# Kernel tuning notes

Measured on AMD Instinct MI355X. Metric: run time of the kernel, lower is better.

## Reference

```python
import jax, jax.numpy as jnp
import numpy as np

N, E = 50000, 800000
D_IN, D_DEG, D_MSG, D_UP, D_H = 128, 16, 128, 128, 256
D = D_IN + D_DEG          # 144, node feature after degree-tag concat
MSG_IN = 2 * D            # 288
UPD_IN = D + D_MSG        # 272

def _mlp_params(key, d_in, d_h, d_out):
    k1, k2 = jax.random.split(key)
    s1 = 1.0 / np.sqrt(d_in)
    s2 = 1.0 / np.sqrt(d_h)
    return (jax.random.uniform(k1, (d_in, d_h), jnp.float32, -s1, s1),
            jnp.zeros((d_h,), jnp.float32),
            jax.random.uniform(k2, (d_h, d_out), jnp.float32, -s2, s2),
            jnp.zeros((d_out,), jnp.float32))

def setup_inputs() -> dict:
    key = jax.random.key(0)
    kx, ke, kd, km, ku = jax.random.split(key, 5)
    x = jax.random.normal(kx, (N, D_IN), jnp.float32)
    edge_index = jax.random.randint(ke, (2, E), 0, N, jnp.int64)
    degrees = jax.random.uniform(kd, (N, D_DEG), jnp.float32)
    mW1, mb1, mW2, mb2 = _mlp_params(km, MSG_IN, D_H, D_MSG)
    uW1, ub1, uW2, ub2 = _mlp_params(ku, UPD_IN, D_H, D_UP)
    return {"x": x, "edge_index": edge_index, "degrees": degrees,
            "msg_W1": mW1, "msg_b1": mb1, "msg_W2": mW2, "msg_b2": mb2,
            "upd_W1": uW1, "upd_b1": ub1, "upd_W2": uW2, "upd_b2": ub2}

def _mlp(h, W1, b1, W2, b2):
    return jax.nn.relu(h @ W1 + b1) @ W2 + b2

def reference(x, edge_index, degrees,
              msg_W1, msg_b1, msg_W2, msg_b2,
              upd_W1, upd_b1, upd_W2, upd_b2):
    # degree_as_tag + retain_features -> concat node features with degree tags
    h = jnp.concatenate([x, degrees], axis=-1)          # [N, D]
    # flow='source_to_target': i = edge_index[1] (target), j = edge_index[0] (source)
    src, tgt = edge_index[0], edge_index[1]
    h_i = h[tgt]                                        # [E, D]
    h_j = h[src]                                        # [E, D]
    msgs = _mlp(jnp.concatenate([h_i, h_j], axis=-1),   # [E, 2D] -> [E, D_MSG]
                msg_W1, msg_b1, msg_W2, msg_b2)
    # sparse sum over source dim == scatter-add onto targets
    agg = jax.ops.segment_sum(msgs, tgt, num_segments=N)  # [N, D_MSG]
    out = _mlp(jnp.concatenate([h, agg], axis=-1),
               upd_W1, upd_b1, upd_W2, upd_b2)          # [N, D_UP]
    return out
```

## Files before the change

kernel.cpp:

```cpp
#include <hip/hip_runtime.h>


#define N_NODES 50000
#define E_EDGES 800000
#define DF   144
#define DIN  128
#define DDEG 16
#define DMSG 128
#define SA_LD 296
#define SH_LD 264
#define PQ_LD 512
#define KA_LD 168
#define EP_W  68
#define ECAP 96
#define OVER_CAP 4096
#define PQ_BLOCKS 782
#define HIST_BLOCKS 3125
#define PACK_THREADS 27648
#define PREP_BLOCKS 3516
#define PACK_BLOCKS 108

typedef __attribute__((ext_vector_type(8))) short short8;
typedef __attribute__((ext_vector_type(4))) float floatx4;
typedef __attribute__((ext_vector_type(4))) unsigned int uintx4;

__device__ __forceinline__ unsigned int fasu(float f){
  union { float f; unsigned int u; } v; v.f = f; return v.u;
}
__device__ __forceinline__ float uasf(unsigned int u){
  union { unsigned int u; float f; } v; v.u = u; return v.f;
}
__device__ __forceinline__ short f2bf(float f){
  unsigned int i = fasu(f);
  unsigned int r = i + 0x7fffu + ((i >> 16) & 1u);
  return (short)(r >> 16);
}
__device__ __forceinline__ unsigned int pk_trunc(float lo, float hi){
  return __builtin_amdgcn_perm(fasu(hi), fasu(lo), 0x07060302u);
}

__global__ void sentinel_kernel(float* __restrict__ out){
  int i = blockIdx.x * blockDim.x + threadIdx.x;
  if (i < N_NODES * DMSG){ out[i] = 2.0f; }
}

__device__ __forceinline__ void pack_w_dev(const float* __restrict__ W,
                                           short* __restrict__ Wp,
                                           int Ksrc, int nT, int t){
  int lane = t & 63;
  int rest = t >> 6;
  int nt = rest % nT;
  int chunk = rest / nT;
  int Ncols = nT * 16;
  int n = nt * 16 + (lane & 15);
  int kbase = chunk * 32 + (lane >> 4) * 8;
  short8 v;
  for (int j = 0; j < 8; ++j){
    int k = kbase + j;
    short o = 0;
    if (k < Ksrc){ o = f2bf(W[(size_t)k * Ncols + n]); }
    v[j] = o;
  }
  *(short8*)(Wp + (size_t)t * 8) = v;
}
__device__ __forceinline__ void pack_w1pq_dev(const float* __restrict__ W1,
                                              short* __restrict__ Wp, int t){
  int lane = t & 63;
  int rest = t >> 6;
  int nt = rest % 32;
  int chunk = rest / 32;
  int col = nt * 16 + (lane & 15);
  int kbase = chunk * 32 + (lane >> 4) * 8;
  short8 v;
  for (int j = 0; j < 8; ++j){
    int k = kbase + j;
    short o = 0;
    if (k < 144){
      float w = (col < 256) ? W1[(size_t)k * 256 + col]
                            : W1[(size_t)(144 + k) * 256 + (col - 256)];
      o = f2bf(w);
    }
    v[j] = o;
  }
  *(short8*)(Wp + (size_t)t * 8) = v;
}

__global__ void prep_pack_kernel(const float* __restrict__ x, const float* __restrict__ deg,
                                 const float* __restrict__ mW1, const float* __restrict__ mW2,
                                 const float* __restrict__ uW1, const float* __restrict__ uW2,
                                 short* __restrict__ w1pq, short* __restrict__ w2m,
                                 short* __restrict__ w1u, short* __restrict__ w2u,
                                 int* __restrict__ cnt, int* __restrict__ nOver,
                                 short* __restrict__ h){
  if (blockIdx.x >= PREP_BLOCKS){
    int t2 = (blockIdx.x - PREP_BLOCKS) * 256 + threadIdx.x;
    if (t2 < 4096){ pack_w_dev(mW2, w2m, 256, 8, t2); }
    else if (t2 < 13312){ pack_w_dev(uW1, w1u, 272, 16, t2 - 4096); }
    else if (t2 < 17408){ pack_w_dev(uW2, w2u, 256, 8, t2 - 13312); }
    else { pack_w1pq_dev(mW1, w1pq, t2 - 17408); }
    return;
  }
  int i = blockIdx.x * 256 + threadIdx.x;
  if (i < N_NODES){ cnt[i] = 0; }
  if (i == 0){ *nOver = 0; }
  if (i < N_NODES * 18){
    int n = i / 18;
    int j = i - n * 18;
    const float* src;
    if (j < 16){ src = x + (size_t)n * DIN + (size_t)j * 8; }
    else       { src = deg + (size_t)n * DDEG + (size_t)(j - 16) * 8; }
    short8 v;
    for (int t = 0; t < 8; ++t){ v[t] = f2bf(src[t]); }
    *(short8*)(h + (size_t)n * DF + (size_t)j * 8) = v;
  }
}

__launch_bounds__(256, 2)
__global__ void pq_scatter_kernel(const short* __restrict__ h, const short* __restrict__ w1pq,
                                  const float* __restrict__ b1, short* __restrict__ PQ,
                                  const int* __restrict__ ei, int* __restrict__ cnt,
                                  int* __restrict__ nOver, unsigned int* __restrict__ over,
                                  unsigned short* __restrict__ es){
  __shared__ __align__(16) unsigned int sE[4 * 32 * EP_W];

  const int g = blockIdx.x;
  const bool isG = ((g % 5) == 0) && ((g / 5) < PQ_BLOCKS);
  if (!isG){
    int nb = (g / 5) + 1; if (nb > PQ_BLOCKS) nb = PQ_BLOCKS;
    int e = (g - nb) * 256 + threadIdx.x;
    if (e < E_EDGES){
      int s = ei[e];
      int t = ei[E_EDGES + e];
      if ((unsigned)s >= (unsigned)N_NODES) s = 0;
      if ((unsigned)t >= (unsigned)N_NODES) t = 0;
      int r = atomicAdd(cnt + t, 1);
      if (r < ECAP){
        es[(size_t)t * ECAP + r] = (unsigned short)s;
      } else {
        int p = atomicAdd(nOver, 1);
        if (p < OVER_CAP){ over[p] = ((unsigned int)t << 16) | (unsigned int)s; }
      }
    }
    return;
  }

  const int tid  = threadIdx.x;
  const int lane = tid & 63;
  const int wave = tid >> 6;
  const int q    = lane >> 4;
  const int lr   = lane & 15;
  const int n0   = (g / 5) * 64;
  short* sA = (short*)sE;

  {
    int row = tid >> 2;
    int quarter = tid & 3;
    int n = n0 + row;
    if (n >= N_NODES) n = 0;
    const short* hp = h + (size_t)n * DF;
    short* dstp = sA + row * KA_LD + quarter * 40;
    #pragma unroll
    for (int c5 = 0; c5 < 5; ++c5){
      int col = quarter * 40 + c5 * 8;
      short8 v;
      if (col < DF){
        v = *(const short8*)(hp + col);
      } else {
        for (int j = 0; j < 8; ++j){ v[j] = 0; }
      }
      *(short8*)(dstp + c5 * 8) = v;
    }
  }
  __syncthreads();

  floatx4 acc[4][8];
  #pragma unroll
  for (int it = 0; it < 4; ++it){
    #pragma unroll
    for (int jt = 0; jt < 8; ++jt){
      #pragma unroll
      for (int r = 0; r < 4; ++r){ acc[it][jt][r] = 0.0f; }
    }
  }

  for (int kc = 0; kc < 5; ++kc){
    short8 aF[4];
    #pragma unroll
    for (int it = 0; it < 4; ++it){
      aF[it] = *(const short8*)(sA + (it * 16 + lr) * KA_LD + kc * 32 + q * 8);
    }
    #pragma unroll
    for (int jt = 0; jt < 8; ++jt){
      short8 bF = *(const short8*)(w1pq + ((size_t)(kc * 32 + wave * 8 + jt) * 64 + lane) * 8);
      #pragma unroll
      for (int it = 0; it < 4; ++it){
        acc[it][jt] = __builtin_amdgcn_mfma_f32_16x16x32_bf16(aF[it], bF, acc[it][jt], 0, 0, 0);
      }
    }
  }
  __syncthreads();

  const int waveBase = wave * (32 * EP_W);
  #pragma unroll
  for (int rnd = 0; rnd < 2; ++rnd){
    #pragma unroll
    for (int il = 0; il < 2; ++il){
      const int it = rnd * 2 + il;
      #pragma unroll
      for (int jt = 0; jt < 8; ++jt){
        int col  = (wave * 8 + jt) * 16 + lr;
        float bb = (col < 256) ? b1[col] : 0.0f;
        floatx4 a = acc[it][jt];
        unsigned int pk01 = pk_trunc(a[0] + bb, a[1] + bb);
        unsigned int pk23 = pk_trunc(a[2] + bb, a[3] + bb);
        unsigned int send = (lr & 1) ? pk01 : pk23;
        unsigned int t = (unsigned int)__shfl_xor((int)send, 1, 64);
        int lrow;
        unsigned int w0, w1;
        if ((lr & 1) == 0){
          lrow = il * 16 + q * 4;
          w0 = (pk01 & 0xffffu) | ((t & 0xffffu) << 16);
          w1 = (pk01 >> 16)     | (t & 0xffff0000u);
        } else {
          lrow = il * 16 + q * 4 + 2;
          w0 = (t & 0xffffu) | ((pk23 & 0xffffu) << 16);
          w1 = (t >> 16)     | (pk23 & 0xffff0000u);
        }
        int wv = jt * 8 + (lr >> 1);
        sE[waveBase + lrow * EP_W + wv] = w0;
        sE[waveBase + (lrow + 1) * EP_W + wv] = w1;
      }
    }
    #pragma unroll
    for (int rr = 0; rr < 8; ++rr){
      int lrow = rr * 4 + (lane >> 4);
      int grow = n0 + rnd * 32 + lrow;
      uintx4 v = *(const uintx4*)(sE + waveBase + lrow * EP_W + (lane & 15) * 4);
      if (grow < N_NODES){
        *(uintx4*)((unsigned int*)PQ + (size_t)grow * 256 + wave * 64 + (lane & 15) * 4) = v;
      }
    }
  }
}

__launch_bounds__(256, 8)
__global__ void hsum_kernel(const short* __restrict__ PQ, const unsigned short* __restrict__ es,
                            const int* __restrict__ cnt, const unsigned int* __restrict__ over,
                            const int* __restrict__ nOver, short* __restrict__ HsumB){
  const int lane = threadIdx.x & 63;
  const int wave = threadIdx.x >> 6;
  const int t = blockIdx.x * 4 + wave;
  const unsigned int* PQu = (const unsigned int*)PQ;

  float a0 = 0.0f, a1 = 0.0f, a2 = 0.0f, a3 = 0.0f;
  int d = cnt[t];
  if (d > 0){
    int dc = d < ECAP ? d : ECAP;
    int start = t * ECAP;
    uint2 pv = *(const uint2*)(PQu + (size_t)t * 256 + lane * 2);
    float Pf0 = uasf(pv.x << 16), Pf1 = uasf(pv.x & 0xffff0000u);
    float Pf2 = uasf(pv.y << 16), Pf3 = uasf(pv.y & 0xffff0000u);

    #define LDQ(idx) (*(const uint2*)(PQu + (size_t)(unsigned int)__shfl((int)el, (idx), 64) * 256 + 128 + lane * 2))
    #define ACCQ(qv) { float v;                                        \
        v = Pf0 + uasf((qv).x << 16);          a0 += v > 0.0f ? v : 0.0f; \
        v = Pf1 + uasf((qv).x & 0xffff0000u);  a1 += v > 0.0f ? v : 0.0f; \
        v = Pf2 + uasf((qv).y << 16);          a2 += v > 0.0f ? v : 0.0f; \
        v = Pf3 + uasf((qv).y & 0xffff0000u);  a3 += v > 0.0f ? v : 0.0f; }

    for (int base = 0; base < dc; base += 64){
      int m = dc - base;
      if (m > 64) m = 64;
      unsigned int el = (lane < m) ? (unsigned int)es[start + base + lane] : 0u;
      uint2 q0 = LDQ(0);
      uint2 q1 = LDQ(1);
      uint2 q2 = LDQ(2);
      uint2 q3 = LDQ(3);
      for (int j = 0; j < m; j += 4){
        uint2 t0 = q0, t1 = q1, t2 = q2, t3 = q3;
        int i0 = j + 4, i1 = j + 5, i2 = j + 6, i3 = j + 7;
        q0 = LDQ(i0 < 64 ? i0 : 0);
        q1 = LDQ(i1 < 64 ? i1 : 0);
        q2 = LDQ(i2 < 64 ? i2 : 0);
        q3 = LDQ(i3 < 64 ? i3 : 0);
        ACCQ(t0);
        if (j + 1 < m){ ACCQ(t1); }
        if (j + 2 < m){ ACCQ(t2); }
        if (j + 3 < m){ ACCQ(t3); }
      }
    }
    #undef LDQ
    #undef ACCQ

    if (d > ECAP){
      int no = *nOver;
      if (no > OVER_CAP) no = OVER_CAP;
      for (int p = 0; p < no; ++p){
        unsigned int w = over[p];
        if ((int)(w >> 16) == t){
          unsigned int s1 = w & 0xffffu;
          uint2 qv = *(const uint2*)(PQu + (size_t)s1 * 256 + 128 + lane * 2);
          float v;
          v = Pf0 + uasf(qv.x << 16);          a0 += v > 0.0f ? v : 0.0f;
          v = Pf1 + uasf(qv.x & 0xffff0000u);  a1 += v > 0.0f ? v : 0.0f;
          v = Pf2 + uasf(qv.y << 16);          a2 += v > 0.0f ? v : 0.0f;
          v = Pf3 + uasf(qv.y & 0xffff0000u);  a3 += v > 0.0f ? v : 0.0f;
        }
      }
    }
  }
  uint2 o;
  o.x = pk_trunc(a0, a1);
  o.y = pk_trunc(a2, a3);
  *(uint2*)((unsigned int*)HsumB + (size_t)t * 128 + lane * 2) = o;
}

__launch_bounds__(256, 4)
__global__ void node2_kernel(const short* __restrict__ h, const short* __restrict__ HsumB,
                             const int* __restrict__ cnt,
                             const short* __restrict__ w2m, const float* __restrict__ b2m,
                             const short* __restrict__ w1u, const float* __restrict__ b1u,
                             const short* __restrict__ w2u, const float* __restrict__ b2u,
                             float* __restrict__ out){
  __shared__ __align__(16) short sBuf[64 * SA_LD];
  __shared__ int sCnt[64];
  const int tid  = threadIdx.x;
  const int lane = tid & 63;
  const int wave = tid >> 6;
  const int q    = lane >> 4;
  const int lr   = lane & 15;
  const int n0   = blockIdx.x * 64;

  {
    int row = tid >> 2;
    int qtr = tid & 3;
    int n = n0 + row; if (n >= N_NODES) n = 0;
    const short* hp = HsumB + (size_t)n * 256 + qtr * 64;
    short* dst = sBuf + row * SA_LD + qtr * 64;
    #pragma unroll
    for (int c = 0; c < 8; ++c){
      *(short8*)(dst + c * 8) = *(const short8*)(hp + c * 8);
    }
    if (tid < 64){
      int n2 = n0 + tid; if (n2 >= N_NODES) n2 = 0;
      sCnt[tid] = cnt[n2];
    }
  }
  __syncthreads();

  floatx4 agga[4][2];
  #pragma unroll
  for (int it = 0; it < 4; ++it){
    #pragma unroll
    for (int jt = 0; jt < 2; ++jt){
      #pragma unroll
      for (int r = 0; r < 4; ++r){ agga[it][jt][r] = 0.0f; }
    }
  }
  for (int kc = 0; kc < 8; ++kc){
    short8 aF[4];
    #pragma unroll
    for (int it = 0; it < 4; ++it){
      aF[it] = *(const short8*)(sBuf + (it * 16 + lr) * SA_LD + kc * 32 + q * 8);
    }
    #pragma unroll
    for (int jt = 0; jt < 2; ++jt){
      short8 bF = *(const short8*)(w2m + ((size_t)(kc * 8 + wave * 2 + jt) * 64 + lane) * 8);
      #pragma unroll
      for (int it = 0; it < 4; ++it){
        agga[it][jt] = __builtin_amdgcn_mfma_f32_16x16x32_bf16(aF[it], bF, agga[it][jt], 0, 0, 0);
      }
    }
  }
  __syncthreads();

  if (tid < 128){
    int row = tid >> 1;
    int half = tid & 1;
    int n = n0 + row; if (n >= N_NODES) n = 0;
    const short* srcp = h + (size_t)n * DF + half * 72;
    short* dstp = sBuf + row * SA_LD + half * 72;
    #pragma unroll
    for (int c = 0; c < 9; ++c){
      *(short8*)(dstp + c * 8) = *(const short8*)(srcp + c * 8);
    }
  } else {
    int t2 = tid - 128;
    int row = t2 >> 1;
    int half = t2 & 1;
    short* padp = sBuf + row * SA_LD + 272 + half * 8;
    #pragma unroll
    for (int t = 0; t < 8; ++t){ padp[t] = 0; }
  }
  #pragma unroll
  for (int jt = 0; jt < 2; ++jt){
    int colm = wave * 32 + jt * 16 + lr;
    int colb = 144 + wave * 32 + jt * 16 + (lr & ~1);
    float bb = b2m[colm];
    #pragma unroll
    for (int it = 0; it < 4; ++it){
      int rb = it * 16 + q * 4;
      float v0 = agga[it][jt][0] + (float)sCnt[rb + 0] * bb;
      float v1 = agga[it][jt][1] + (float)sCnt[rb + 1] * bb;
      float v2 = agga[it][jt][2] + (float)sCnt[rb + 2] * bb;
      float v3 = agga[it][jt][3] + (float)sCnt[rb + 3] * bb;
      unsigned int pk01 = pk_trunc(v0, v1);
      unsigned int pk23 = pk_trunc(v2, v3);
      unsigned int send = (lr & 1) ? pk01 : pk23;
      unsigned int t = (unsigned int)__shfl_xor((int)send, 1, 64);
      int row0;
      unsigned int w0, w1;
      if ((lr & 1) == 0){
        row0 = rb;
        w0 = (pk01 & 0xffffu) | ((t & 0xffffu) << 16);
        w1 = (pk01 >> 16)     | (t & 0xffff0000u);
      } else {
        row0 = rb + 2;
        w0 = (t & 0xffffu) | ((pk23 & 0xffffu) << 16);
        w1 = (t >> 16)     | (pk23 & 0xffff0000u);
      }
      *(unsigned int*)(sBuf + row0 * SA_LD + colb) = w0;
      *(unsigned int*)(sBuf + (row0 + 1) * SA_LD + colb) = w1;
    }
  }
  __syncthreads();

  floatx4 acc[4][4];
  #pragma unroll
  for (int it = 0; it < 4; ++it){
    #pragma unroll
    for (int jt = 0; jt < 4; ++jt){
      #pragma unroll
      for (int r = 0; r < 4; ++r){ acc[it][jt][r] = 0.0f; }
    }
  }
  for (int kc = 0; kc < 9; ++kc){
    short8 aF[4];
    #pragma unroll
    for (int it = 0; it < 4; ++it){
      aF[it] = *(const short8*)(sBuf + (it * 16 + lr) * SA_LD + kc * 32 + q * 8);
    }
    #pragma unroll
    for (int jt = 0; jt < 4; ++jt){
      short8 bF = *(const short8*)(w1u + ((size_t)(kc * 16 + wave * 4 + jt) * 64 + lane) * 8);
      #pragma unroll
      for (int it = 0; it < 4; ++it){
        acc[it][jt] = __builtin_amdgcn_mfma_f32_16x16x32_bf16(aF[it], bF, acc[it][jt], 0, 0, 0);
      }
    }
  }
  __syncthreads();
  #pragma unroll
  for (int jt = 0; jt < 4; ++jt){
    int col  = wave * 64 + jt * 16 + lr;
    int colb = wave * 64 + jt * 16 + (lr & ~1);
    float bb = b1u[col];
    #pragma unroll
    for (int it = 0; it < 4; ++it){
      floatx4 a = acc[it][jt];
      float v0 = a[0] + bb; v0 = v0 > 0.0f ? v0 : 0.0f;
      float v1 = a[1] + bb; v1 = v1 > 0.0f ? v1 : 0.0f;
      float v2 = a[2] + bb; v2 = v2 > 0.0f ? v2 : 0.0f;
      float v3 = a[3] + bb; v3 = v3 > 0.0f ? v3 : 0.0f;
      unsigned int pk01 = pk_trunc(v0, v1);
      unsigned int pk23 = pk_trunc(v2, v3);
      unsigned int send = (lr & 1) ? pk01 : pk23;
      unsigned int t = (unsigned int)__shfl_xor((int)send, 1, 64);
      int row0;
      unsigned int w0, w1;
      if ((lr & 1) == 0){
        row0 = it * 16 + q * 4;
        w0 = (pk01 & 0xffffu) | ((t & 0xffffu) << 16);
        w1 = (pk01 >> 16)     | (t & 0xffff0000u);
      } else {
        row0 = it * 16 + q * 4 + 2;
        w0 = (t & 0xffffu) | ((pk23 & 0xffffu) << 16);
        w1 = (t >> 16)     | (pk23 & 0xffff0000u);
      }
      *(unsigned int*)(sBuf + row0 * SH_LD + colb) = w0;
      *(unsigned int*)(sBuf + (row0 + 1) * SH_LD + colb) = w1;
    }
  }
  __syncthreads();

  floatx4 acc2[4][2];
  #pragma unroll
  for (int it = 0; it < 4; ++it){
    #pragma unroll
    for (int jt = 0; jt < 2; ++jt){
      #pragma unroll
      for (int r = 0; r < 4; ++r){ acc2[it][jt][r] = 0.0f; }
    }
  }
  for (int kc = 0; kc < 8; ++kc){
    short8 aF[4];
    #pragma unroll
    for (int it = 0; it < 4; ++it){
      aF[it] = *(const short8*)(sBuf + (it * 16 + lr) * SH_LD + kc * 32 + q * 8);
    }
    #pragma unroll
    for (int jt = 0; jt < 2; ++jt){
      short8 bF = *(const short8*)(w2u + ((size_t)(kc * 8 + wave * 2 + jt) * 64 + lane) * 8);
      #pragma unroll
      for (int it = 0; it < 4; ++it){
        acc2[it][jt] = __builtin_amdgcn_mfma_f32_16x16x32_bf16(aF[it], bF, acc2[it][jt], 0, 0, 0);
      }
    }
  }
  __syncthreads();
  float* sO = (float*)sBuf;
  #pragma unroll
  for (int jt = 0; jt < 2; ++jt){
    int col = wave * 32 + jt * 16 + lr;
    float bb = b2u[col];
    #pragma unroll
    for (int it = 0; it < 4; ++it){
      #pragma unroll
      for (int r = 0; r < 4; ++r){
        sO[(it * 16 + q * 4 + r) * 132 + col] = acc2[it][jt][r] + bb;
      }
    }
  }
  __syncthreads();
  #pragma unroll
  for (int rr = 0; rr < 8; ++rr){
    int row = rr * 8 + (tid >> 5);
    int n = n0 + row;
    if (n < N_NODES){
      *(floatx4*)(out + (size_t)n * DMSG + (tid & 31) * 4) =
          *(const floatx4*)(sO + row * 132 + (tid & 31) * 4);
    }
  }
}

extern "C" void kernel_launch(void* const* d_in, const int* in_sizes, int n_in,
                              void* d_out, int out_size, void* d_ws, size_t ws_size,
                              hipStream_t stream){
  const float* x   = (const float*)d_in[0];
  const int*   ei  = (const int*)d_in[1];
  const float* deg = (const float*)d_in[2];
  const float* mW1 = (const float*)d_in[3];
  const float* mb1 = (const float*)d_in[4];
  const float* mW2 = (const float*)d_in[5];
  const float* mb2 = (const float*)d_in[6];
  const float* uW1 = (const float*)d_in[7];
  const float* ub1 = (const float*)d_in[8];
  const float* uW2 = (const float*)d_in[9];
  const float* ub2 = (const float*)d_in[10];

  char* ws = (char*)d_ws;
  size_t off = 0;
  short* HsumB = (short*)(ws + off); off += (size_t)N_NODES * 256 * 2;
  short* hbuf  = (short*)(ws + off); off += (size_t)N_NODES * DF * 2;
  off = (off + 255) & ~(size_t)255;
  short* w2m  = (short*)(ws + off); off += (size_t)8 * 8 * 64 * 8 * 2;
  short* w1u  = (short*)(ws + off); off += (size_t)9 * 16 * 64 * 8 * 2;
  short* w2u  = (short*)(ws + off); off += (size_t)8 * 8 * 64 * 8 * 2;
  short* w1pq = (short*)(ws + off); off += (size_t)5 * 32 * 64 * 8 * 2;
  off = (off + 255) & ~(size_t)255;
  short* PQ = (short*)(ws + off); off += (size_t)N_NODES * PQ_LD * 2;
  unsigned short* es = (unsigned short*)(ws + off); off += (size_t)N_NODES * ECAP * 2;
  int* cnt   = (int*)(ws + off); off += (size_t)N_NODES * 4;
  int* nOver = (int*)(ws + off); off += 256;
  unsigned int* over = (unsigned int*)(ws + off); off += (size_t)OVER_CAP * 4;

  if (ws_size < off){
    sentinel_kernel<<<(N_NODES * DMSG + 255) / 256, 256, 0, stream>>>((float*)d_out);
    return;
  }

  prep_pack_kernel<<<PREP_BLOCKS + PACK_BLOCKS, 256, 0, stream>>>(
      x, deg, mW1, mW2, uW1, uW2, w1pq, w2m, w1u, w2u, cnt, nOver, hbuf);
  pq_scatter_kernel<<<PQ_BLOCKS + HIST_BLOCKS, 256, 0, stream>>>(
      hbuf, w1pq, mb1, PQ, ei, cnt, nOver, over, es);
  hsum_kernel<<<(N_NODES + 3) / 4, 256, 0, stream>>>(PQ, es, cnt, over, nOver, HsumB);
  node2_kernel<<<(N_NODES + 63) / 64, 256, 0, stream>>>(hbuf, HsumB, cnt, w2m, mb2,
                                                        w1u, ub1, w2u, ub2,
                                                        (float*)d_out);
}
```

Baseline: 256.3 us.

## Shard edge bucketing counters per XCD with workgroup-scope atomics

Each XCD now gets its own copy of the per-target counter and edge-slot arrays, chosen from the hardware XCC_ID register. Counter increments use relaxed atomics instead of device-wide atomics, which aims to cut cross-die contention and coherence traffic in the scatter phase. The hsum kernel merges the eight sub-buckets using prefix offsets and writes a total degree array for the node kernel. The workgroup memory scope is relied on to be correct because each XCD only touches its own shard. Per-shard capacity is small (16), so high-degree nodes may spill into the serial overflow list more often.

```diff
diff --git a/kernel.cpp b/kernel.cpp
--- a/kernel.cpp
+++ b/kernel.cpp
@@ -12,11 +12,11 @@
 #define PQ_LD 512
 #define KA_LD 168
 #define EP_W  68
-#define ECAP 96
+#define NSLOT 50176
+#define CAP8  16
 #define OVER_CAP 4096
 #define PQ_BLOCKS 782
 #define HIST_BLOCKS 3125
-#define PACK_THREADS 27648
 #define PREP_BLOCKS 3516
 #define PACK_BLOCKS 108
 
@@ -90,7 +90,7 @@
                                  const float* __restrict__ uW1, const float* __restrict__ uW2,
                                  short* __restrict__ w1pq, short* __restrict__ w2m,
                                  short* __restrict__ w1u, short* __restrict__ w2u,
-                                 int* __restrict__ cnt, int* __restrict__ nOver,
+                                 int* __restrict__ cnt8, int* __restrict__ nOver,
                                  short* __restrict__ h){
   if (blockIdx.x >= PREP_BLOCKS){
     int t2 = (blockIdx.x - PREP_BLOCKS) * 256 + threadIdx.x;
@@ -101,7 +101,7 @@
     return;
   }
   int i = blockIdx.x * 256 + threadIdx.x;
-  if (i < N_NODES){ cnt[i] = 0; }
+  if (i < 8 * NSLOT){ cnt8[i] = 0; }
   if (i == 0){ *nOver = 0; }
   if (i < N_NODES * 18){
     int n = i / 18;
@@ -118,14 +118,17 @@
 __launch_bounds__(256, 2)
 __global__ void pq_scatter_kernel(const short* __restrict__ h, const short* __restrict__ w1pq,
                                   const float* __restrict__ b1, short* __restrict__ PQ,
-                                  const int* __restrict__ ei, int* __restrict__ cnt,
+                                  const int* __restrict__ ei, int* __restrict__ cnt8,
                                   int* __restrict__ nOver, unsigned int* __restrict__ over,
-                                  unsigned short* __restrict__ es){
+                                  unsigned short* __restrict__ es8){
   __shared__ __align__(16) unsigned int sE[4 * 32 * EP_W];
 
   const int g = blockIdx.x;
   const bool isG = ((g % 5) == 0) && ((g / 5) < PQ_BLOCKS);
   if (!isG){
+    unsigned int xcd;
+    asm("s_getreg_b32 %0, hwreg(HW_REG_XCC_ID, 0, 32)" : "=s"(xcd));
+    xcd &= 7u;
     int nb = (g / 5) + 1; if (nb > PQ_BLOCKS) nb = PQ_BLOCKS;
     int e = (g - nb) * 256 + threadIdx.x;
     if (e < E_EDGES){
@@ -133,9 +136,10 @@
       int t = ei[E_EDGES + e];
       if ((unsigned)s >= (unsigned)N_NODES) s = 0;
       if ((unsigned)t >= (unsigned)N_NODES) t = 0;
-      int r = atomicAdd(cnt + t, 1);
-      if (r < ECAP){
-        es[(size_t)t * ECAP + r] = (unsigned short)s;
+      int* cp = cnt8 + (size_t)xcd * NSLOT + t;
+      int r = __hip_atomic_fetch_add(cp, 1, __ATOMIC_RELAXED, __HIP_MEMORY_SCOPE_WORKGROUP);
+      if (r < CAP8){
+        es8[((size_t)xcd * N_NODES + t) * CAP8 + r] = (unsigned short)s;
       } else {
         int p = atomicAdd(nOver, 1);
         if (p < OVER_CAP){ over[p] = ((unsigned int)t << 16) | (unsigned int)s; }
@@ -244,71 +248,81 @@
 }
 
 __launch_bounds__(256, 8)
-__global__ void hsum_kernel(const short* __restrict__ PQ, const unsigned short* __restrict__ es,
-                            const int* __restrict__ cnt, const unsigned int* __restrict__ over,
-                            const int* __restrict__ nOver, short* __restrict__ HsumB){
+__global__ void hsum_kernel(const short* __restrict__ PQ, const unsigned short* __restrict__ es8,
+                            const int* __restrict__ cnt8, const unsigned int* __restrict__ over,
+                            const int* __restrict__ nOver, short* __restrict__ HsumB,
+                            int* __restrict__ dtot){
   const int lane = threadIdx.x & 63;
   const int wave = threadIdx.x >> 6;
   const int t = blockIdx.x * 4 + wave;
   const unsigned int* PQu = (const unsigned int*)PQ;
 
+  uint2 pv = *(const uint2*)(PQu + (size_t)t * 256 + lane * 2);
+  int craw = (lane < 8) ? cnt8[(size_t)lane * NSLOT + t] : 0;
+  int cc = craw < CAP8 ? craw : CAP8;
+
+  int c0 = __shfl(cc, 0, 64), c1 = __shfl(cc, 1, 64), c2 = __shfl(cc, 2, 64), c3 = __shfl(cc, 3, 64);
+  int c4 = __shfl(cc, 4, 64), c5 = __shfl(cc, 5, 64), c6 = __shfl(cc, 6, 64), c7 = __shfl(cc, 7, 64);
+  int dtrue = __shfl(craw, 0, 64) + __shfl(craw, 1, 64) + __shfl(craw, 2, 64) + __shfl(craw, 3, 64)
+            + __shfl(craw, 4, 64) + __shfl(craw, 5, 64) + __shfl(craw, 6, 64) + __shfl(craw, 7, 64);
+  int e1 = c0, e2 = e1 + c1, e3 = e2 + c2, e4 = e3 + c3;
+  int e5 = e4 + c4, e6 = e5 + c5, e7 = e6 + c6, e8 = e7 + c7;
+  if (lane == 0){ dtot[t] = dtrue; }
+
   float a0 = 0.0f, a1 = 0.0f, a2 = 0.0f, a3 = 0.0f;
-  int d = cnt[t];
-  if (d > 0){
-    int dc = d < ECAP ? d : ECAP;
-    int start = t * ECAP;
-    uint2 pv = *(const uint2*)(PQu + (size_t)t * 256 + lane * 2);
-    float Pf0 = uasf(pv.x << 16), Pf1 = uasf(pv.x & 0xffff0000u);
-    float Pf2 = uasf(pv.y << 16), Pf3 = uasf(pv.y & 0xffff0000u);
-
-    #define LDQ(idx) (*(const uint2*)(PQu + (size_t)(unsigned int)__shfl((int)el, (idx), 64) * 256 + 128 + lane * 2))
-    #define ACCQ(qv) { float v;                                        \
-        v = Pf0 + uasf((qv).x << 16);          a0 += v > 0.0f ? v : 0.0f; \
-        v = Pf1 + uasf((qv).x & 0xffff0000u);  a1 += v > 0.0f ? v : 0.0f; \
-        v = Pf2 + uasf((qv).y << 16);          a2 += v > 0.0f ? v : 0.0f; \
-        v = Pf3 + uasf((qv).y & 0xffff0000u);  a3 += v > 0.0f ? v : 0.0f; }
-
-    for (int base = 0; base < dc; base += 64){
-      int m = dc - base;
-      if (m > 64) m = 64;
-      unsigned int el = (lane < m) ? (unsigned int)es[start + base + lane] : 0u;
-      uint2 q0 = LDQ(0);
-      uint2 q1 = LDQ(1);
-      uint2 q2 = LDQ(2);
-      uint2 q3 = LDQ(3);
-      for (int j = 0; j < m; j += 4){
-        uint2 t0 = q0, t1 = q1, t2 = q2, t3 = q3;
-        int i0 = j + 4, i1 = j + 5, i2 = j + 6, i3 = j + 7;
-        q0 = LDQ(i0 < 64 ? i0 : 0);
-        q1 = LDQ(i1 < 64 ? i1 : 0);
-        q2 = LDQ(i2 < 64 ? i2 : 0);
-        q3 = LDQ(i3 < 64 ? i3 : 0);
-        ACCQ(t0);
-        if (j + 1 < m){ ACCQ(t1); }
-        if (j + 2 < m){ ACCQ(t2); }
-        if (j + 3 < m){ ACCQ(t3); }
-      }
-    }
-    #undef LDQ
-    #undef ACCQ
-
-    if (d > ECAP){
-      int no = *nOver;
-      if (no > OVER_CAP) no = OVER_CAP;
-      for (int p = 0; p < no; ++p){
-        unsigned int w = over[p];
-        if ((int)(w >> 16) == t){
-          unsigned int s1 = w & 0xffffu;
-          uint2 qv = *(const uint2*)(PQu + (size_t)s1 * 256 + 128 + lane * 2);
-          float v;
-          v = Pf0 + uasf(qv.x << 16);          a0 += v > 0.0f ? v : 0.0f;
-          v = Pf1 + uasf(qv.x & 0xffff0000u);  a1 += v > 0.0f ? v : 0.0f;
-          v = Pf2 + uasf(qv.y << 16);          a2 += v > 0.0f ? v : 0.0f;
-          v = Pf3 + uasf(qv.y & 0xffff0000u);  a3 += v > 0.0f ? v : 0.0f;
-        }
-      }
-    }
-  }
+  float Pf0 = uasf(pv.x << 16), Pf1 = uasf(pv.x & 0xffff0000u);
+  float Pf2 = uasf(pv.y << 16), Pf3 = uasf(pv.y & 0xffff0000u);
+
+  #define LDQ(idx) (*(const uint2*)(PQu + (size_t)(unsigned int)__shfl((int)el, (idx), 64) * 256 + 128 + lane * 2))
+  #define ACCQ(qv) { float v;                                        \
+      v = Pf0 + uasf((qv).x << 16);          a0 += v > 0.0f ? v : 0.0f; \
+      v = Pf1 + uasf((qv).x & 0xffff0000u);  a1 += v > 0.0f ? v : 0.0f; \
+      v = Pf2 + uasf((qv).y << 16);          a2 += v > 0.0f ? v : 0.0f; \
+      v = Pf3 + uasf((qv).y & 0xffff0000u);  a3 += v > 0.0f ? v : 0.0f; }
+
+  for (int base = 0; base < e8; base += 64){
+    int m = e8 - base; if (m > 64) m = 64;
+    int jj = base + lane;
+    int f1 = jj >= e1, f2 = jj >= e2, f3 = jj >= e3, f4 = jj >= e4;
+    int f5 = jj >= e5, f6 = jj >= e6, f7 = jj >= e7;
+    int x  = f1 + f2 + f3 + f4 + f5 + f6 + f7;
+    int ex = (f1 ? c0 : 0) + (f2 ? c1 : 0) + (f3 ? c2 : 0) + (f4 ? c3 : 0)
+           + (f5 ? c4 : 0) + (f6 ? c5 : 0) + (f7 ? c6 : 0);
+    unsigned int el = (jj < e8)
+        ? (unsigned int)es8[((size_t)x * N_NODES + t) * CAP8 + (jj - ex)] : 0u;
+    uint2 q0 = LDQ(0);
+    uint2 q1 = LDQ(1);
+    uint2 q2 = LDQ(2);
+    uint2 q3 = LDQ(3);
+    for (int j = 0; j < m; j += 4){
+      uint2 t0 = q0, t1 = q1, t2 = q2, t3 = q3;
+      int i0 = j + 4, i1 = j + 5, i2 = j + 6, i3 = j + 7;
+      q0 = LDQ(i0 < 64 ? i0 : 0);
+      q1 = LDQ(i1 < 64 ? i1 : 0);
+      q2 = LDQ(i2 < 64 ? i2 : 0);
+      q3 = LDQ(i3 < 64 ? i3 : 0);
+      ACCQ(t0);
+      if (j + 1 < m){ ACCQ(t1); }
+      if (j + 2 < m){ ACCQ(t2); }
+      if (j + 3 < m){ ACCQ(t3); }
+    }
+  }
+
+  if (dtrue > e8){
+    int no = *nOver;
+    if (no > OVER_CAP) no = OVER_CAP;
+    for (int p = 0; p < no; ++p){
+      unsigned int w = over[p];
+      if ((int)(w >> 16) == t){
+        unsigned int s1 = w & 0xffffu;
+        uint2 qv = *(const uint2*)(PQu + (size_t)s1 * 256 + 128 + lane * 2);
+        ACCQ(qv);
+      }
+    }
+  }
+  #undef ACCQ
+  #undef LDQ
+
   uint2 o;
   o.x = pk_trunc(a0, a1);
   o.y = pk_trunc(a2, a3);
@@ -317,7 +331,7 @@
 
 __launch_bounds__(256, 4)
 __global__ void node2_kernel(const short* __restrict__ h, const short* __restrict__ HsumB,
-                             const int* __restrict__ cnt,
+                             const int* __restrict__ dtot,
                              const short* __restrict__ w2m, const float* __restrict__ b2m,
                              const short* __restrict__ w1u, const float* __restrict__ b1u,
                              const short* __restrict__ w2u, const float* __restrict__ b2u,
@@ -343,7 +357,7 @@
     }
     if (tid < 64){
       int n2 = n0 + tid; if (n2 >= N_NODES) n2 = 0;
-      sCnt[tid] = cnt[n2];
+      sCnt[tid] = dtot[n2];
     }
   }
   __syncthreads();
@@ -559,8 +573,11 @@
   short* w1pq = (short*)(ws + off); off += (size_t)5 * 32 * 64 * 8 * 2;
   off = (off + 255) & ~(size_t)255;
   short* PQ = (short*)(ws + off); off += (size_t)N_NODES * PQ_LD * 2;
-  unsigned short* es = (unsigned short*)(ws + off); off += (size_t)N_NODES * ECAP * 2;
-  int* cnt   = (int*)(ws + off); off += (size_t)N_NODES * 4;
+  unsigned short* es8 = (unsigned short*)(ws + off);
+  off += (size_t)8 * N_NODES * CAP8 * 2;
+  off = (off + 255) & ~(size_t)255;
+  int* cnt8 = (int*)(ws + off); off += (size_t)8 * NSLOT * 4;
+  int* dtot = (int*)(ws + off); off += (size_t)NSLOT * 4;
   int* nOver = (int*)(ws + off); off += 256;
   unsigned int* over = (unsigned int*)(ws + off); off += (size_t)OVER_CAP * 4;
 
@@ -570,11 +587,11 @@
   }
 
   prep_pack_kernel<<<PREP_BLOCKS + PACK_BLOCKS, 256, 0, stream>>>(
-      x, deg, mW1, mW2, uW1, uW2, w1pq, w2m, w1u, w2u, cnt, nOver, hbuf);
+      x, deg, mW1, mW2, uW1, uW2, w1pq, w2m, w1u, w2u, cnt8, nOver, hbuf);
   pq_scatter_kernel<<<PQ_BLOCKS + HIST_BLOCKS, 256, 0, stream>>>(
-      hbuf, w1pq, mb1, PQ, ei, cnt, nOver, over, es);
-  hsum_kernel<<<(N_NODES + 3) / 4, 256, 0, stream>>>(PQ, es, cnt, over, nOver, HsumB);
-  node2_kernel<<<(N_NODES + 63) / 64, 256, 0, stream>>>(hbuf, HsumB, cnt, w2m, mb2,
+      hbuf, w1pq, mb1, PQ, ei, cnt8, nOver, over, es8);
+  hsum_kernel<<<(N_NODES + 3) / 4, 256, 0, stream>>>(PQ, es8, cnt8, over, nOver, HsumB, dtot);
+  node2_kernel<<<(N_NODES + 63) / 64, 256, 0, stream>>>(hbuf, HsumB, dtot, w2m, mb2,
                                                         w1u, ub1, w2u, ub2,
                                                         (float*)d_out);
 }
```

Result: no change. 256.0 us (median of 2 runs) (-0.1%).
